# Kernel tuning notes

Measured on AMD Instinct MI355X. Metric: run time of the kernel, lower is better.

The kernel has to match this reference:

```python
import jax, jax.numpy as jnp
import numpy as np

RHO = 1060.0   # blood density kg/m^3
DX = 1e-3      # grid spacing
CCFL = 0.9     # CFL number
EPS_A = 1e-6   # area floor


def setup_inputs() -> dict:
    key = jax.random.key(0)
    k0, k1, k2 = jax.random.split(key, 3)
    M = 90000          # 3 vessels x 30000 cells
    T = 150            # time steps
    Rs = jax.random.normal(k0, (4,), dtype=jnp.float32)
    sim_dat = jnp.ones((2, M), dtype=jnp.float32)            # row0: A, row1: Q seed
    sim_dat_const = jax.random.uniform(k1, (11, M), dtype=jnp.float32)
    input_data = jax.random.uniform(k2, (T,), dtype=jnp.float32)
    strides = jnp.array([[0, 30000], [30000, 60000], [60000, 90000]], dtype=jnp.int32)
    return {"Rs": Rs, "sim_dat": sim_dat, "sim_dat_const": sim_dat_const,
            "input_data": input_data, "strides": strides, "upper": T}


def reference(Rs, sim_dat, sim_dat_const, input_data, strides, upper):
    M = sim_dat.shape[1]
    # --- SimDense: softplus reparam of 4 resistance scale factors ---
    rs = jax.nn.softplus(Rs)
    idx = jnp.arange(M)
    m1 = (idx >= strides[1, 0]) & (idx < strides[1, 1])  # vessel 1 region
    m2 = (idx >= strides[2, 0]) & (idx < strides[2, 1])  # vessel 2 region
    # constant rows (shifted positive)
    A0 = sim_dat_const[0] + 0.5     # reference area
    beta = sim_dat_const[1] + 1.0   # wall stiffness
    R1 = sim_dat_const[7] + 0.5     # proximal resistance (VAR_INDEX_1)
    R2 = sim_dat_const[8] + 0.5     # distal resistance (VAR_INDEX_2)
    # scatter scaled resistances into vessel-1 / vessel-2 regions
    R1 = jnp.where(m1, rs[0] * R1, jnp.where(m2, rs[2] * R1, R1))
    R2 = jnp.where(m1, rs[1] * R2, jnp.where(m2, rs[3] * R2, R2))
    Rtot = R1 + R2

    A_init = sim_dat[0]
    Q_init = 0.1 * sim_dat[1]
    starts = strides[:, 0]
    ends = strides[:, 1] - 1
    mids = (strides[:, 0] + strides[:, 1]) // 2

    def step(carry, inflow):
        A, Q = carry
        A = jnp.maximum(A, EPS_A)
        sq = jnp.sqrt(A / A0)
        P = beta * (sq - 1.0)                 # tube-law pressure
        u = Q / A
        c = jnp.sqrt(0.5 * beta / RHO * sq)   # wave speed
        smax = jnp.max(jnp.abs(u) + c)
        dt = CCFL * DX / smax                 # CFL-limited timestep
        # conservative fluxes for (A, Q)
        F_A = Q
        F_Q = Q * u + beta / (3.0 * RHO * A0) * A * sq
        # Lax-Friedrichs interface fluxes
        fhA = 0.5 * (F_A[:-1] + F_A[1:]) - 0.5 * smax * (A[1:] - A[:-1])
        fhQ = 0.5 * (F_Q[:-1] + F_Q[1:]) - 0.5 * smax * (Q[1:] - Q[:-1])
        lam = dt / DX
        A_new = A.at[1:-1].add(-lam * (fhA[1:] - fhA[:-1]))
        Q_new = Q.at[1:-1].add(-lam * (fhQ[1:] - fhQ[:-1]))
        # inlet / junction BC: prescribed inflow at each vessel start
        Q_new = Q_new.at[starts].set(inflow)
        # outlet BC: resistive Windkessel Q = P / (R1 + R2)
        Q_new = Q_new.at[ends].set(P[ends] / Rtot[ends])
        A_new = jnp.maximum(A_new, EPS_A)
        return (A_new, Q_new), P[mids]          # record mid-vessel pressures

    _, p = jax.lax.scan(step, (A_init, Q_init), input_data)
    return p  # [upper, 3]
```

## Files before the change

### kernel.cpp

```cpp
#include <hip/hip_runtime.h>

static constexpr int MM  = 90000;
static constexpr int TT  = 150;
static constexpr int BS  = 256;
static constexpr int CPT = 4;
static constexpr int CPB = BS * CPT;
static constexpr int NB  = (MM + CPB - 1) / CPB;
static constexpr int WPB = BS / 64;
static constexpr int PAGE_U32 = 2048;
static constexpr int PAGE_U64 = 1024;

__device__ unsigned int       g_bmax_s[128][PAGE_U32];
__device__ unsigned long long g_edge_s[NB][PAGE_U64];
__device__ unsigned long long g_dummy64;

__device__ __forceinline__ float softplus_f(float x) {
    return fmaxf(x, 0.0f) + log1pf(expf(-fabsf(x)));
}
__device__ __forceinline__ unsigned long long packAQ(float A, float Q) {
    return ((unsigned long long)__float_as_uint(Q) << 32) | (unsigned long long)__float_as_uint(A);
}
#define AG_LOAD32(p)     __hip_atomic_load((p), __ATOMIC_RELAXED, __HIP_MEMORY_SCOPE_AGENT)
#define AG_LOAD64(p)     __hip_atomic_load((p), __ATOMIC_RELAXED, __HIP_MEMORY_SCOPE_AGENT)
#define AG_STORE32(p, v) __hip_atomic_store((p), (v), __ATOMIC_RELAXED, __HIP_MEMORY_SCOPE_AGENT)
#define AG_STORE64(p, v) __hip_atomic_store((p), (v), __ATOMIC_RELAXED, __HIP_MEMORY_SCOPE_AGENT)

__global__ void init_ws_kernel() {
    int i = blockIdx.x * blockDim.x + threadIdx.x;
    int stride = gridDim.x * blockDim.x;
    unsigned int* pb = &g_bmax_s[0][0];
    for (int j = i; j < 128 * PAGE_U32; j += stride)
        pb[j] = ((j / PAGE_U32) < NB) ? 0u : 1u;
    unsigned long long* pe = &g_edge_s[0][0];
    for (int j = i; j < NB * PAGE_U64; j += stride) pe[j] = 0ull;
    if (i == 0) g_dummy64 = ~0ull;
}

__global__ void __launch_bounds__(BS) sim_kernel(
    const float* __restrict__ Rs,
    const float* __restrict__ sim_dat,
    const float* __restrict__ sdc,
    const float* __restrict__ inflow,
    float* __restrict__ out)
{
    __shared__ float sE[2][WPB][2][3];
    __shared__ float sred[2][WPB];
    __shared__ float s_smaxv;
    __shared__ float s_hL[3], s_hR[3];
    __shared__ float s_inflow[TT];

    const int b    = blockIdx.x;
    const int tid  = threadIdx.x;
    const int wv   = tid >> 6;
    const int lane = tid & 63;
    const int base = b * CPB + tid * CPT;

    for (int j = tid; j < TT; j += BS) s_inflow[j] = inflow[j];

    float A[CPT], Q[CPT], A0v[CPT], bet[CPT], cbv[CPT], k2v[CPT], sq[CPT], FQ[CPT];
    bool  act[CPT];
    #pragma unroll
    for (int c = 0; c < CPT; ++c) {
        int i = base + c;
        act[c] = (i < MM);
        if (act[c]) {
            A[c]   = fmaxf(sim_dat[i], 1e-6f);
            Q[c]   = 0.1f * sim_dat[MM + i];
            A0v[c] = sdc[i] + 0.5f;
            bet[c] = sdc[MM + i] + 1.0f;
        } else { A[c] = 1.0f; Q[c] = 0.0f; A0v[c] = 1.0f; bet[c] = 1.0f; }
        cbv[c] = (0.5f * bet[c]) / 1060.0f;
        k2v[c] = bet[c] / (3180.0f * A0v[c]);
    }
    const bool isStart = (base == 0) | (base == 30000) | (base == 60000);
    const bool isEnd   = (base + 3 == 29999) | (base + 3 == 59999) | (base + 3 == 89999);
    const int midSlot = (base == 15000) ? 0 : (base == 45000) ? 1 : (base == 75000) ? 2 : -1;
    float Rtot = 1.0f;
    if (isEnd) {
        int i3 = base + 3;
        float R1 = sdc[7 * MM + i3] + 0.5f;
        float R2 = sdc[8 * MM + i3] + 0.5f;
        if (i3 == 59999)      { R1 *= softplus_f(Rs[0]); R2 *= softplus_f(Rs[1]); }
        else if (i3 == 89999) { R1 *= softplus_f(Rs[2]); R2 *= softplus_f(Rs[3]); }
        Rtot = R1 + R2;
    }

    const bool pubL = (tid == 0) && (b > 0);
    const bool pubR = (tid == BS - 1) && (b < NB - 1);
    const bool fixL = pubL;
    const bool fixR = pubR;

    float s4 = 0.0f;
    #pragma unroll
    for (int c = 0; c < CPT; ++c) {
        sq[c] = sqrtf(A[c] / A0v[c]);
        float u  = Q[c] / A[c];
        float cc = sqrtf(cbv[c] * sq[c]);
        FQ[c] = Q[c] * u + k2v[c] * A[c] * sq[c];
        s4 = fmaxf(s4, act[c] ? (fabsf(u) + cc) : 0.0f);
    }
    if (pubL) {
        AG_STORE64(&g_edge_s[b][0], packAQ(A[0], Q[0]));
        AG_STORE64(&g_edge_s[b][1], (unsigned long long)__float_as_uint(FQ[0]));
    }
    if (pubR) {
        AG_STORE64(&g_edge_s[b][2], packAQ(A[3], Q[3]));
        AG_STORE64(&g_edge_s[b][3], (unsigned long long)__float_as_uint(FQ[3]));
    }
    {
        float mm = s4;
        #pragma unroll
        for (int off = 32; off > 0; off >>= 1) mm = fmaxf(mm, __shfl_xor(mm, off, 64));
        if (lane == 0)       { sE[0][wv][0][0] = A[0]; sE[0][wv][0][1] = Q[0]; sE[0][wv][0][2] = FQ[0];
                               sred[0][wv] = mm; }
        else if (lane == 63) { sE[0][wv][1][0] = A[3]; sE[0][wv][1][1] = Q[3]; sE[0][wv][1][2] = FQ[3]; }
    }
    __syncthreads();
    if (wv == 0 && lane == 0) {
        float bm = fmaxf(fmaxf(sred[0][0], sred[0][1]), fmaxf(sred[0][2], sred[0][3]));
        AG_STORE32(&g_bmax_s[b][0], __float_as_uint(bm));
    }

    for (int t = 0; t < TT; ++t) {
        const int par = t & 1, npar = par ^ 1;

        float Am = __shfl_up(A[3], 1, 64),  Qm = __shfl_up(Q[3], 1, 64),  Fm = __shfl_up(FQ[3], 1, 64);
        float Ap = __shfl_down(A[0], 1, 64), Qp = __shfl_down(Q[0], 1, 64), Fp = __shfl_down(FQ[0], 1, 64);
        if (lane == 0 && wv > 0)       { Am = sE[par][wv-1][1][0]; Qm = sE[par][wv-1][1][1]; Fm = sE[par][wv-1][1][2]; }
        if (lane == 63 && wv < WPB - 1){ Ap = sE[par][wv+1][0][0]; Qp = sE[par][wv+1][0][1]; Fp = sE[par][wv+1][0][2]; }

        float dFA[CPT], lapA[CPT], dFQ[CPT], lapQ[CPT];
        #pragma unroll
        for (int c = 0; c < CPT; ++c) {
            float Al = (c == 0) ? Am : A[c-1],  Ql = (c == 0) ? Qm : Q[c-1],  Fl = (c == 0) ? Fm : FQ[c-1];
            float Ar = (c == 3) ? Ap : A[c+1],  Qr = (c == 3) ? Qp : Q[c+1],  Fr = (c == 3) ? Fp : FQ[c+1];
            dFA[c]  = 0.5f * (Qr - Ql);
            lapA[c] = 0.5f * (Ar - 2.0f * A[c] + Al);
            dFQ[c]  = 0.5f * (Fr - Fl);
            lapQ[c] = 0.5f * (Qr - 2.0f * Q[c] + Ql);
        }
        if (midSlot >= 0) out[t * 3 + midSlot] = bet[0] * (sq[0] - 1.0f);
        const float Pend = bet[3] * (sq[3] - 1.0f);

        if (wv == 0) {
            const unsigned long long* pE = &g_dummy64;
            const int t4 = t * 4;
            if (lane == 0 && b > 0)           pE = &g_edge_s[b - 1][t4 + 2];
            else if (lane == 1 && b > 0)      pE = &g_edge_s[b - 1][t4 + 3];
            else if (lane == 2 && b < NB - 1) pE = &g_edge_s[b + 1][t4 + 0];
            else if (lane == 3 && b < NB - 1) pE = &g_edge_s[b + 1][t4 + 1];
            unsigned int x0, x1;
            unsigned long long e64;
            for (;;) {
                x0  = AG_LOAD32(&g_bmax_s[lane][t]);
                x1  = AG_LOAD32(&g_bmax_s[64 + lane][t]);
                e64 = AG_LOAD64(pE);
                if (__all((x0 != 0u) & (x1 != 0u) & (e64 != 0ull))) break;
            }
            float ml = fmaxf(__uint_as_float(x0), __uint_as_float(x1));
            #pragma unroll
            for (int off = 32; off > 0; off >>= 1) ml = fmaxf(ml, __shfl_xor(ml, off, 64));
            if (lane == 0) s_smaxv = ml;
            if (lane == 0 && b > 0)           { s_hL[0] = __uint_as_float((unsigned int)e64);
                                                s_hL[1] = __uint_as_float((unsigned int)(e64 >> 32)); }
            else if (lane == 1 && b > 0)      { s_hL[2] = __uint_as_float((unsigned int)e64); }
            else if (lane == 2 && b < NB - 1) { s_hR[0] = __uint_as_float((unsigned int)e64);
                                                s_hR[1] = __uint_as_float((unsigned int)(e64 >> 32)); }
            else if (lane == 3 && b < NB - 1) { s_hR[2] = __uint_as_float((unsigned int)e64); }
        }
        __syncthreads();

        const float smax = s_smaxv;
        const float dt  = ((float)(0.9 * 0.001)) / smax;
        const float lam = dt / 0.001f;
        const float w   = lam * smax;

        if (fixL) {
            float Al = s_hL[0], Ql = s_hL[1], Fl = s_hL[2];
            dFA[0]  = 0.5f * (Q[1] - Ql);
            lapA[0] = 0.5f * (A[1] - 2.0f * A[0] + Al);
            dFQ[0]  = 0.5f * (FQ[1] - Fl);
            lapQ[0] = 0.5f * (Q[1] - 2.0f * Q[0] + Ql);
        }
        if (fixR) {
            float Ar = s_hR[0], Qr = s_hR[1], Fr = s_hR[2];
            dFA[3]  = 0.5f * (Qr - Q[2]);
            lapA[3] = 0.5f * (Ar - 2.0f * A[3] + A[2]);
            dFQ[3]  = 0.5f * (Fr - FQ[2]);
            lapQ[3] = 0.5f * (Qr - 2.0f * Q[3] + Q[2]);
        }
        #pragma unroll
        for (int c = 0; c < CPT; ++c) {
            int i = base + c;
            if (act[c] && i > 0 && i < MM - 1) {
                A[c] = fmaf(w, lapA[c], fmaf(-lam, dFA[c], A[c]));
                Q[c] = fmaf(w, lapQ[c], fmaf(-lam, dFQ[c], Q[c]));
            }
        }
        if (isStart) Q[0] = s_inflow[t];
        if (isEnd)   Q[3] = Pend / Rtot;
        #pragma unroll
        for (int c = 0; c < CPT; ++c) A[c] = fmaxf(A[c], 1e-6f);

        const int n4 = (t + 1) * 4;
        if (pubL) AG_STORE64(&g_edge_s[b][n4 + 0], packAQ(A[0], Q[0]));
        if (pubR) AG_STORE64(&g_edge_s[b][n4 + 2], packAQ(A[3], Q[3]));

        s4 = 0.0f;
        #pragma unroll
        for (int c = 0; c < CPT; ++c) {
            sq[c] = sqrtf(A[c] / A0v[c]);
            float u  = Q[c] / A[c];
            float cc = sqrtf(cbv[c] * sq[c]);
            FQ[c] = Q[c] * u + k2v[c] * A[c] * sq[c];
            s4 = fmaxf(s4, act[c] ? (fabsf(u) + cc) : 0.0f);
        }
        if (pubL) AG_STORE64(&g_edge_s[b][n4 + 1], (unsigned long long)__float_as_uint(FQ[0]));
        if (pubR) AG_STORE64(&g_edge_s[b][n4 + 3], (unsigned long long)__float_as_uint(FQ[3]));

        float mm = s4;
        #pragma unroll
        for (int off = 32; off > 0; off >>= 1) mm = fmaxf(mm, __shfl_xor(mm, off, 64));
        if (lane == 0)       { sE[npar][wv][0][0] = A[0]; sE[npar][wv][0][1] = Q[0]; sE[npar][wv][0][2] = FQ[0];
                               sred[npar][wv] = mm; }
        else if (lane == 63) { sE[npar][wv][1][0] = A[3]; sE[npar][wv][1][1] = Q[3]; sE[npar][wv][1][2] = FQ[3]; }
        __syncthreads();

        if (wv == 0 && lane == 0) {
            float bm = fmaxf(fmaxf(sred[npar][0], sred[npar][1]), fmaxf(sred[npar][2], sred[npar][3]));
            AG_STORE32(&g_bmax_s[b][t + 1], __float_as_uint(bm));
        }
    }
}

extern "C" void kernel_launch(void* const* d_in, const int* in_sizes, int n_in,
                              void* d_out, int out_size, void* d_ws, size_t ws_size,
                              hipStream_t stream) {
    (void)in_sizes; (void)n_in; (void)d_ws; (void)ws_size; (void)out_size;

    const float* Rs      = (const float*)d_in[0];
    const float* sim_dat = (const float*)d_in[1];
    const float* sdc     = (const float*)d_in[2];
    const float* inflow  = (const float*)d_in[3];
    float* out = (float*)d_out;

    hipLaunchKernelGGL(init_ws_kernel, dim3(240), dim3(256), 0, stream);

    hipLaunchKernelGGL(sim_kernel, dim3(NB), dim3(BS), 0, stream,
                       Rs, sim_dat, sdc, inflow, out);
}
```

Before: 480.9 us.

## Publish per-wave maxima globally and replace mid-step barrier with LDS flag polling

Each wave now writes its own max wave speed straight to global memory, so the per-block reduction and the barrier before publishing are gone. Wave 0 polls all per-wave slots across the grid and hands smax to the other waves through an LDS flag instead of a __syncthreads. The last wave of each block polls the right-neighbour halo itself. This shortens the critical path between a block finishing a step and its neighbours seeing its results, at the cost of 4x more global max reads per poll and spinning waves that compete for issue slots.

```diff
diff --git a/kernel.cpp b/kernel.cpp
--- a/kernel.cpp
+++ b/kernel.cpp
@@ -7,10 +7,9 @@
 static constexpr int CPB = BS * CPT;
 static constexpr int NB  = (MM + CPB - 1) / CPB;
 static constexpr int WPB = BS / 64;
-static constexpr int PAGE_U32 = 2048;
 static constexpr int PAGE_U64 = 1024;
 
-__device__ unsigned int       g_bmax_s[128][PAGE_U32];
+__device__ unsigned long long g_wmax_s[128][PAGE_U64];
 __device__ unsigned long long g_edge_s[NB][PAGE_U64];
 __device__ unsigned long long g_dummy64;
 
@@ -20,7 +19,6 @@
 __device__ __forceinline__ unsigned long long packAQ(float A, float Q) {
     return ((unsigned long long)__float_as_uint(Q) << 32) | (unsigned long long)__float_as_uint(A);
 }
-#define AG_LOAD32(p)     __hip_atomic_load((p), __ATOMIC_RELAXED, __HIP_MEMORY_SCOPE_AGENT)
 #define AG_LOAD64(p)     __hip_atomic_load((p), __ATOMIC_RELAXED, __HIP_MEMORY_SCOPE_AGENT)
 #define AG_STORE32(p, v) __hip_atomic_store((p), (v), __ATOMIC_RELAXED, __HIP_MEMORY_SCOPE_AGENT)
 #define AG_STORE64(p, v) __hip_atomic_store((p), (v), __ATOMIC_RELAXED, __HIP_MEMORY_SCOPE_AGENT)
@@ -28,9 +26,9 @@
 __global__ void init_ws_kernel() {
     int i = blockIdx.x * blockDim.x + threadIdx.x;
     int stride = gridDim.x * blockDim.x;
-    unsigned int* pb = &g_bmax_s[0][0];
-    for (int j = i; j < 128 * PAGE_U32; j += stride)
-        pb[j] = ((j / PAGE_U32) < NB) ? 0u : 1u;
+    unsigned long long* pw = &g_wmax_s[0][0];
+    for (int j = i; j < 128 * PAGE_U64; j += stride)
+        pw[j] = ((j / PAGE_U64) < NB) ? 0ull : 0x0000000100000001ull;
     unsigned long long* pe = &g_edge_s[0][0];
     for (int j = i; j < NB * PAGE_U64; j += stride) pe[j] = 0ull;
     if (i == 0) g_dummy64 = ~0ull;
@@ -43,11 +41,9 @@
     const float* __restrict__ inflow,
     float* __restrict__ out)
 {
-    __shared__ float sE[2][WPB][2][3];
-    __shared__ float sred[2][WPB];
-    __shared__ float s_smaxv;
-    __shared__ float s_hL[3], s_hR[3];
-    __shared__ float s_inflow[TT];
+    __shared__ float        sE[2][WPB][2][3];
+    __shared__ unsigned int s_smax[TT + 1];
+    __shared__ float        s_inflow[TT];
 
     const int b    = blockIdx.x;
     const int tid  = threadIdx.x;
@@ -56,6 +52,7 @@
     const int base = b * CPB + tid * CPT;
 
     for (int j = tid; j < TT; j += BS) s_inflow[j] = inflow[j];
+    for (int j = tid; j <= TT; j += BS) s_smax[j] = 0u;
 
     float A[CPT], Q[CPT], A0v[CPT], bet[CPT], cbv[CPT], k2v[CPT], sq[CPT], FQ[CPT];
     bool  act[CPT];
@@ -112,17 +109,15 @@
         #pragma unroll
         for (int off = 32; off > 0; off >>= 1) mm = fmaxf(mm, __shfl_xor(mm, off, 64));
         if (lane == 0)       { sE[0][wv][0][0] = A[0]; sE[0][wv][0][1] = Q[0]; sE[0][wv][0][2] = FQ[0];
-                               sred[0][wv] = mm; }
+                               AG_STORE32((unsigned int*)&g_wmax_s[b][0] + wv, __float_as_uint(mm)); }
         else if (lane == 63) { sE[0][wv][1][0] = A[3]; sE[0][wv][1][1] = Q[3]; sE[0][wv][1][2] = FQ[3]; }
     }
     __syncthreads();
-    if (wv == 0 && lane == 0) {
-        float bm = fmaxf(fmaxf(sred[0][0], sred[0][1]), fmaxf(sred[0][2], sred[0][3]));
-        AG_STORE32(&g_bmax_s[b][0], __float_as_uint(bm));
-    }
 
     for (int t = 0; t < TT; ++t) {
         const int par = t & 1, npar = par ^ 1;
+        const int t4 = t * 4;
+        const int t2 = t * 2;
 
         float Am = __shfl_up(A[3], 1, 64),  Qm = __shfl_up(Q[3], 1, 64),  Fm = __shfl_up(FQ[3], 1, 64);
         float Ap = __shfl_down(A[0], 1, 64), Qp = __shfl_down(Q[0], 1, 64), Fp = __shfl_down(FQ[0], 1, 64);
@@ -142,52 +137,77 @@
         if (midSlot >= 0) out[t * 3 + midSlot] = bet[0] * (sq[0] - 1.0f);
         const float Pend = bet[3] * (sq[3] - 1.0f);
 
+        float smax;
+        float hA = 1.0f, hQ = 0.0f, hF = 1.0f;
         if (wv == 0) {
-            const unsigned long long* pE = &g_dummy64;
-            const int t4 = t * 4;
-            if (lane == 0 && b > 0)           pE = &g_edge_s[b - 1][t4 + 2];
-            else if (lane == 1 && b > 0)      pE = &g_edge_s[b - 1][t4 + 3];
-            else if (lane == 2 && b < NB - 1) pE = &g_edge_s[b + 1][t4 + 0];
-            else if (lane == 3 && b < NB - 1) pE = &g_edge_s[b + 1][t4 + 1];
-            unsigned int x0, x1;
-            unsigned long long e64;
+            const unsigned long long* pA = &g_dummy64;
+            const unsigned long long* pF = &g_dummy64;
+            if (lane == 0 && b > 0) { pA = &g_edge_s[b - 1][t4 + 2]; pF = &g_edge_s[b - 1][t4 + 3]; }
+            unsigned long long v0, v1, v2, v3, eA, eF;
             for (;;) {
-                x0  = AG_LOAD32(&g_bmax_s[lane][t]);
-                x1  = AG_LOAD32(&g_bmax_s[64 + lane][t]);
-                e64 = AG_LOAD64(pE);
-                if (__all((x0 != 0u) & (x1 != 0u) & (e64 != 0ull))) break;
-            }
-            float ml = fmaxf(__uint_as_float(x0), __uint_as_float(x1));
+                v0 = AG_LOAD64(&g_wmax_s[lane][t2]);
+                v1 = AG_LOAD64(&g_wmax_s[lane][t2 + 1]);
+                v2 = AG_LOAD64(&g_wmax_s[64 + lane][t2]);
+                v3 = AG_LOAD64(&g_wmax_s[64 + lane][t2 + 1]);
+                eA = AG_LOAD64(pA);
+                eF = AG_LOAD64(pF);
+                bool ok = ((unsigned int)v0 != 0u) & ((unsigned int)(v0 >> 32) != 0u)
+                        & ((unsigned int)v1 != 0u) & ((unsigned int)(v1 >> 32) != 0u)
+                        & ((unsigned int)v2 != 0u) & ((unsigned int)(v2 >> 32) != 0u)
+                        & ((unsigned int)v3 != 0u) & ((unsigned int)(v3 >> 32) != 0u)
+                        & (eA != 0ull) & (eF != 0ull);
+                if (__all(ok)) break;
+            }
+            float ml = fmaxf(
+                fmaxf(fmaxf(__uint_as_float((unsigned int)v0), __uint_as_float((unsigned int)(v0 >> 32))),
+                      fmaxf(__uint_as_float((unsigned int)v1), __uint_as_float((unsigned int)(v1 >> 32)))),
+                fmaxf(fmaxf(__uint_as_float((unsigned int)v2), __uint_as_float((unsigned int)(v2 >> 32))),
+                      fmaxf(__uint_as_float((unsigned int)v3), __uint_as_float((unsigned int)(v3 >> 32)))));
             #pragma unroll
             for (int off = 32; off > 0; off >>= 1) ml = fmaxf(ml, __shfl_xor(ml, off, 64));
-            if (lane == 0) s_smaxv = ml;
-            if (lane == 0 && b > 0)           { s_hL[0] = __uint_as_float((unsigned int)e64);
-                                                s_hL[1] = __uint_as_float((unsigned int)(e64 >> 32)); }
-            else if (lane == 1 && b > 0)      { s_hL[2] = __uint_as_float((unsigned int)e64); }
-            else if (lane == 2 && b < NB - 1) { s_hR[0] = __uint_as_float((unsigned int)e64);
-                                                s_hR[1] = __uint_as_float((unsigned int)(e64 >> 32)); }
-            else if (lane == 3 && b < NB - 1) { s_hR[2] = __uint_as_float((unsigned int)e64); }
-        }
-        __syncthreads();
-
-        const float smax = s_smaxv;
+            smax = ml;
+            if (lane == 0) {
+                __hip_atomic_store(&s_smax[t], __float_as_uint(ml),
+                                   __ATOMIC_RELAXED, __HIP_MEMORY_SCOPE_WORKGROUP);
+                hA = __uint_as_float((unsigned int)eA);
+                hQ = __uint_as_float((unsigned int)(eA >> 32));
+                hF = __uint_as_float((unsigned int)eF);
+            }
+        } else {
+            const unsigned long long* pA = &g_dummy64;
+            const unsigned long long* pF = &g_dummy64;
+            if (wv == WPB - 1 && lane == 63 && b < NB - 1) {
+                pA = &g_edge_s[b + 1][t4 + 0]; pF = &g_edge_s[b + 1][t4 + 1];
+            }
+            unsigned int sm;
+            unsigned long long eA, eF;
+            for (;;) {
+                sm = __hip_atomic_load(&s_smax[t], __ATOMIC_RELAXED, __HIP_MEMORY_SCOPE_WORKGROUP);
+                eA = AG_LOAD64(pA);
+                eF = AG_LOAD64(pF);
+                if (__all((sm != 0u) & (eA != 0ull) & (eF != 0ull))) break;
+            }
+            smax = __uint_as_float(sm);
+            hA = __uint_as_float((unsigned int)eA);
+            hQ = __uint_as_float((unsigned int)(eA >> 32));
+            hF = __uint_as_float((unsigned int)eF);
+        }
+
         const float dt  = ((float)(0.9 * 0.001)) / smax;
         const float lam = dt / 0.001f;
         const float w   = lam * smax;
 
         if (fixL) {
-            float Al = s_hL[0], Ql = s_hL[1], Fl = s_hL[2];
-            dFA[0]  = 0.5f * (Q[1] - Ql);
-            lapA[0] = 0.5f * (A[1] - 2.0f * A[0] + Al);
-            dFQ[0]  = 0.5f * (FQ[1] - Fl);
-            lapQ[0] = 0.5f * (Q[1] - 2.0f * Q[0] + Ql);
+            dFA[0]  = 0.5f * (Q[1] - hQ);
+            lapA[0] = 0.5f * (A[1] - 2.0f * A[0] + hA);
+            dFQ[0]  = 0.5f * (FQ[1] - hF);
+            lapQ[0] = 0.5f * (Q[1] - 2.0f * Q[0] + hQ);
         }
         if (fixR) {
-            float Ar = s_hR[0], Qr = s_hR[1], Fr = s_hR[2];
-            dFA[3]  = 0.5f * (Qr - Q[2]);
-            lapA[3] = 0.5f * (Ar - 2.0f * A[3] + A[2]);
-            dFQ[3]  = 0.5f * (Fr - FQ[2]);
-            lapQ[3] = 0.5f * (Qr - 2.0f * Q[3] + Q[2]);
+            dFA[3]  = 0.5f * (hQ - Q[2]);
+            lapA[3] = 0.5f * (hA - 2.0f * A[3] + A[2]);
+            dFQ[3]  = 0.5f * (hF - FQ[2]);
+            lapQ[3] = 0.5f * (hQ - 2.0f * Q[3] + Q[2]);
         }
         #pragma unroll
         for (int c = 0; c < CPT; ++c) {
@@ -202,7 +222,7 @@
         #pragma unroll
         for (int c = 0; c < CPT; ++c) A[c] = fmaxf(A[c], 1e-6f);
 
-        const int n4 = (t + 1) * 4;
+        const int n4 = t4 + 4;
         if (pubL) AG_STORE64(&g_edge_s[b][n4 + 0], packAQ(A[0], Q[0]));
         if (pubR) AG_STORE64(&g_edge_s[b][n4 + 2], packAQ(A[3], Q[3]));
 
@@ -222,14 +242,10 @@
         #pragma unroll
         for (int off = 32; off > 0; off >>= 1) mm = fmaxf(mm, __shfl_xor(mm, off, 64));
         if (lane == 0)       { sE[npar][wv][0][0] = A[0]; sE[npar][wv][0][1] = Q[0]; sE[npar][wv][0][2] = FQ[0];
-                               sred[npar][wv] = mm; }
+                               AG_STORE32((unsigned int*)&g_wmax_s[b][t2 + 2] + wv, __float_as_uint(mm)); }
         else if (lane == 63) { sE[npar][wv][1][0] = A[3]; sE[npar][wv][1][1] = Q[3]; sE[npar][wv][1][2] = FQ[3]; }
+
         __syncthreads();
-
-        if (wv == 0 && lane == 0) {
-            float bm = fmaxf(fmaxf(sred[npar][0], sred[npar][1]), fmaxf(sred[npar][2], sred[npar][3]));
-            AG_STORE32(&g_bmax_s[b][t + 1], __float_as_uint(bm));
-        }
     }
 }
 
```

After: 546.7 us. 1.14x slower.

## Replace per-step barriers with LDS atomic flags and publish edge flux early

Applied to the files above, without the earlier changes.

Drops one __syncthreads per step. Wave 0 now hands smax to the other waves through a per-step LDS flag that they spin on, and the block max is reduced with LDS atomicMax plus a counter so the last-arriving wave publishes it globally. Edge cells recompute their flux right away so neighbour blocks get A, Q and F before the full-cell update runs. The aim is to shorten the cross-block critical path, at the cost of extra LDS atomics, spin-waiting and a little duplicated sqrt and divide work.

```diff
diff --git a/kernel.cpp b/kernel.cpp
--- a/kernel.cpp
+++ b/kernel.cpp
@@ -24,6 +24,7 @@
 #define AG_LOAD64(p)     __hip_atomic_load((p), __ATOMIC_RELAXED, __HIP_MEMORY_SCOPE_AGENT)
 #define AG_STORE32(p, v) __hip_atomic_store((p), (v), __ATOMIC_RELAXED, __HIP_MEMORY_SCOPE_AGENT)
 #define AG_STORE64(p, v) __hip_atomic_store((p), (v), __ATOMIC_RELAXED, __HIP_MEMORY_SCOPE_AGENT)
+#define LDS_WAIT()       asm volatile("s_waitcnt lgkmcnt(0)" ::: "memory")
 
 __global__ void init_ws_kernel() {
     int i = blockIdx.x * blockDim.x + threadIdx.x;
@@ -43,11 +44,12 @@
     const float* __restrict__ inflow,
     float* __restrict__ out)
 {
-    __shared__ float sE[2][WPB][2][3];
-    __shared__ float sred[2][WPB];
-    __shared__ float s_smaxv;
-    __shared__ float s_hL[3], s_hR[3];
-    __shared__ float s_inflow[TT];
+    __shared__ float        sE[2][WPB][2][3];
+    __shared__ unsigned int lds_bmax[TT + 1];
+    __shared__ unsigned int lds_cnt[TT + 1];
+    __shared__ unsigned int s_smax[TT + 1];
+    __shared__ float        s_hL[3], s_hR[3];
+    __shared__ float        s_inflow[TT];
 
     const int b    = blockIdx.x;
     const int tid  = threadIdx.x;
@@ -56,6 +58,7 @@
     const int base = b * CPB + tid * CPT;
 
     for (int j = tid; j < TT; j += BS) s_inflow[j] = inflow[j];
+    for (int j = tid; j <= TT; j += BS) { lds_bmax[j] = 0u; lds_cnt[j] = 0u; s_smax[j] = 0u; }
 
     float A[CPT], Q[CPT], A0v[CPT], bet[CPT], cbv[CPT], k2v[CPT], sq[CPT], FQ[CPT];
     bool  act[CPT];
@@ -90,6 +93,8 @@
     const bool fixL = pubL;
     const bool fixR = pubR;
 
+    __syncthreads();
+
     float s4 = 0.0f;
     #pragma unroll
     for (int c = 0; c < CPT; ++c) {
@@ -111,18 +116,23 @@
         float mm = s4;
         #pragma unroll
         for (int off = 32; off > 0; off >>= 1) mm = fmaxf(mm, __shfl_xor(mm, off, 64));
-        if (lane == 0)       { sE[0][wv][0][0] = A[0]; sE[0][wv][0][1] = Q[0]; sE[0][wv][0][2] = FQ[0];
-                               sred[0][wv] = mm; }
+        if (lane == 0)       { sE[0][wv][0][0] = A[0]; sE[0][wv][0][1] = Q[0]; sE[0][wv][0][2] = FQ[0]; }
         else if (lane == 63) { sE[0][wv][1][0] = A[3]; sE[0][wv][1][1] = Q[3]; sE[0][wv][1][2] = FQ[3]; }
+        if (lane == 0) {
+            atomicMax(&lds_bmax[0], __float_as_uint(mm));
+            LDS_WAIT();
+            unsigned int old = atomicAdd(&lds_cnt[0], 1u);
+            if (old == WPB - 1) {
+                unsigned int bm = __hip_atomic_load(&lds_bmax[0], __ATOMIC_RELAXED, __HIP_MEMORY_SCOPE_WORKGROUP);
+                AG_STORE32(&g_bmax_s[b][0], bm);
+            }
+        }
     }
     __syncthreads();
-    if (wv == 0 && lane == 0) {
-        float bm = fmaxf(fmaxf(sred[0][0], sred[0][1]), fmaxf(sred[0][2], sred[0][3]));
-        AG_STORE32(&g_bmax_s[b][0], __float_as_uint(bm));
-    }
 
     for (int t = 0; t < TT; ++t) {
         const int par = t & 1, npar = par ^ 1;
+        const int t4 = t * 4;
 
         float Am = __shfl_up(A[3], 1, 64),  Qm = __shfl_up(Q[3], 1, 64),  Fm = __shfl_up(FQ[3], 1, 64);
         float Ap = __shfl_down(A[0], 1, 64), Qp = __shfl_down(Q[0], 1, 64), Fp = __shfl_down(FQ[0], 1, 64);
@@ -142,9 +152,9 @@
         if (midSlot >= 0) out[t * 3 + midSlot] = bet[0] * (sq[0] - 1.0f);
         const float Pend = bet[3] * (sq[3] - 1.0f);
 
+        float smax;
         if (wv == 0) {
             const unsigned long long* pE = &g_dummy64;
-            const int t4 = t * 4;
             if (lane == 0 && b > 0)           pE = &g_edge_s[b - 1][t4 + 2];
             else if (lane == 1 && b > 0)      pE = &g_edge_s[b - 1][t4 + 3];
             else if (lane == 2 && b < NB - 1) pE = &g_edge_s[b + 1][t4 + 0];
@@ -160,17 +170,25 @@
             float ml = fmaxf(__uint_as_float(x0), __uint_as_float(x1));
             #pragma unroll
             for (int off = 32; off > 0; off >>= 1) ml = fmaxf(ml, __shfl_xor(ml, off, 64));
-            if (lane == 0) s_smaxv = ml;
+            smax = ml;
             if (lane == 0 && b > 0)           { s_hL[0] = __uint_as_float((unsigned int)e64);
                                                 s_hL[1] = __uint_as_float((unsigned int)(e64 >> 32)); }
             else if (lane == 1 && b > 0)      { s_hL[2] = __uint_as_float((unsigned int)e64); }
             else if (lane == 2 && b < NB - 1) { s_hR[0] = __uint_as_float((unsigned int)e64);
                                                 s_hR[1] = __uint_as_float((unsigned int)(e64 >> 32)); }
             else if (lane == 3 && b < NB - 1) { s_hR[2] = __uint_as_float((unsigned int)e64); }
-        }
-        __syncthreads();
-
-        const float smax = s_smaxv;
+            LDS_WAIT();
+            if (lane == 0)
+                __hip_atomic_store(&s_smax[t], __float_as_uint(ml),
+                                   __ATOMIC_RELAXED, __HIP_MEMORY_SCOPE_WORKGROUP);
+        } else {
+            unsigned int sm;
+            do {
+                sm = __hip_atomic_load(&s_smax[t], __ATOMIC_RELAXED, __HIP_MEMORY_SCOPE_WORKGROUP);
+            } while (sm == 0u);
+            smax = __uint_as_float(sm);
+        }
+
         const float dt  = ((float)(0.9 * 0.001)) / smax;
         const float lam = dt / 0.001f;
         const float w   = lam * smax;
@@ -202,9 +220,21 @@
         #pragma unroll
         for (int c = 0; c < CPT; ++c) A[c] = fmaxf(A[c], 1e-6f);
 
-        const int n4 = (t + 1) * 4;
-        if (pubL) AG_STORE64(&g_edge_s[b][n4 + 0], packAQ(A[0], Q[0]));
-        if (pubR) AG_STORE64(&g_edge_s[b][n4 + 2], packAQ(A[3], Q[3]));
+        const int n4 = t4 + 4;
+        if (pubL) {
+            float sqe = sqrtf(A[0] / A0v[0]);
+            float ue  = Q[0] / A[0];
+            float Fe  = Q[0] * ue + k2v[0] * A[0] * sqe;
+            AG_STORE64(&g_edge_s[b][n4 + 0], packAQ(A[0], Q[0]));
+            AG_STORE64(&g_edge_s[b][n4 + 1], (unsigned long long)__float_as_uint(Fe));
+        }
+        if (pubR) {
+            float sqe = sqrtf(A[3] / A0v[3]);
+            float ue  = Q[3] / A[3];
+            float Fe  = Q[3] * ue + k2v[3] * A[3] * sqe;
+            AG_STORE64(&g_edge_s[b][n4 + 2], packAQ(A[3], Q[3]));
+            AG_STORE64(&g_edge_s[b][n4 + 3], (unsigned long long)__float_as_uint(Fe));
+        }
 
         s4 = 0.0f;
         #pragma unroll
@@ -215,21 +245,23 @@
             FQ[c] = Q[c] * u + k2v[c] * A[c] * sq[c];
             s4 = fmaxf(s4, act[c] ? (fabsf(u) + cc) : 0.0f);
         }
-        if (pubL) AG_STORE64(&g_edge_s[b][n4 + 1], (unsigned long long)__float_as_uint(FQ[0]));
-        if (pubR) AG_STORE64(&g_edge_s[b][n4 + 3], (unsigned long long)__float_as_uint(FQ[3]));
-
         float mm = s4;
         #pragma unroll
         for (int off = 32; off > 0; off >>= 1) mm = fmaxf(mm, __shfl_xor(mm, off, 64));
-        if (lane == 0)       { sE[npar][wv][0][0] = A[0]; sE[npar][wv][0][1] = Q[0]; sE[npar][wv][0][2] = FQ[0];
-                               sred[npar][wv] = mm; }
+        if (lane == 0)       { sE[npar][wv][0][0] = A[0]; sE[npar][wv][0][1] = Q[0]; sE[npar][wv][0][2] = FQ[0]; }
         else if (lane == 63) { sE[npar][wv][1][0] = A[3]; sE[npar][wv][1][1] = Q[3]; sE[npar][wv][1][2] = FQ[3]; }
+
+        if (lane == 0) {
+            atomicMax(&lds_bmax[t + 1], __float_as_uint(mm));
+            LDS_WAIT();
+            unsigned int old = atomicAdd(&lds_cnt[t + 1], 1u);
+            if (old == WPB - 1) {
+                unsigned int bm = __hip_atomic_load(&lds_bmax[t + 1], __ATOMIC_RELAXED, __HIP_MEMORY_SCOPE_WORKGROUP);
+                AG_STORE32(&g_bmax_s[b][t + 1], bm);
+            }
+        }
+
         __syncthreads();
-
-        if (wv == 0 && lane == 0) {
-            float bm = fmaxf(fmaxf(sred[npar][0], sred[npar][1]), fmaxf(sred[npar][2], sred[npar][3]));
-            AG_STORE32(&g_bmax_s[b][t + 1], __float_as_uint(bm));
-        }
     }
 }
 
```

After: 488.9 us. No clear change (+1.7%).
